# Kernel tuning notes

Measured on AMD Instinct MI355X. Metric: run time of the kernel, lower is better.

Reference implementation:

```python
import jax, jax.numpy as jnp
import numpy as np

B, L, D, H = 8, 512, 512, 8  # d_keys = d_values = d_model = D (default path)


def setup_inputs() -> dict:
    key = jax.random.key(0)
    ks = jax.random.split(key, 9)
    w = 0.02
    return {
        "queries": jax.random.normal(ks[0], (B, L, D), dtype=jnp.float32),
        "keys": jax.random.normal(ks[1], (B, L, D), dtype=jnp.float32),
        "values": jax.random.normal(ks[2], (B, L, D), dtype=jnp.float32),
        "Wq": jax.random.normal(ks[3], (D, D * H), dtype=jnp.float32) * w,
        "bq": jnp.zeros((D * H,), dtype=jnp.float32),
        "Wk": jax.random.normal(ks[4], (D, D * H), dtype=jnp.float32) * w,
        "bk": jnp.zeros((D * H,), dtype=jnp.float32),
        "Wv": jax.random.normal(ks[5], (D, D * H), dtype=jnp.float32) * w,
        "bv": jnp.zeros((D * H,), dtype=jnp.float32),
        "attn_mask": 0,  # must be falsy; original code would crash on a real tensor mask
    }


def reference(queries, keys, values, Wq, bq, Wk, bk, Wv, bv, attn_mask):
    b, l, d = queries.shape
    h = Wq.shape[1] // d
    # projections -> (B, L, H, E) with E = d_model
    q = (queries @ Wq + bq).reshape(b, l, h, d)
    k = (keys @ Wk + bk).reshape(b, l, h, d)
    v = (values @ Wv + bv).reshape(b, l, h, d)
    scale = 1.0 / np.sqrt(d).astype(np.float32)
    # per-position head-vs-head scores (B, L, H, H); equivalent to the i-loop
    s = jnp.einsum('blhe,blge->blhg', q, k) * scale
    p = jax.nn.softmax(s, axis=-1)
    # diagonal (l == i) contribution, summed over positions -> (B, H, E)
    attn_part = jnp.einsum('blhg,blge->bhe', p, v)
    # off-diagonal (l != i): uniform 1/H softmax of zero scores, (L-1) copies
    uniform_part = (jnp.float32(l - 1) / h) * v.sum(axis=(1, 2))  # (B, E)
    out = attn_part + uniform_part[:, None, :]  # (B, H, E)
    # final view(B, L, -1): requires L | H*E
    return out.reshape(b, l, -1)
```

## Files before the change

### kernel.cpp

```cpp
#include <hip/hip_runtime.h>


using bf16x8 = __attribute__((ext_vector_type(8))) short;
using f32x4  = __attribute__((ext_vector_type(4))) float;

__device__ __forceinline__ unsigned short f2bf(float f) {
    union { float f; unsigned int u; } c; c.f = f;
    unsigned int u = c.u;
    u += 0x7FFFu + ((u >> 16) & 1u);
    return (unsigned short)(u >> 16);
}
__device__ __forceinline__ float bflo(unsigned int u) {
    union { unsigned int u; float f; } c; c.u = u << 16; return c.f;
}
__device__ __forceinline__ float bfhi(unsigned int u) {
    union { unsigned int u; float f; } c; c.u = u & 0xFFFF0000u; return c.f;
}

#define GLOAD16(gp, lp) __builtin_amdgcn_global_load_lds( \
    (const __attribute__((address_space(1))) unsigned int*)(gp), \
    (__attribute__((address_space(3))) unsigned int*)(lp), 16, 0, 0)

__global__ __launch_bounds__(256) void prep(
    const float* __restrict__ x0, const float* __restrict__ x1,
    unsigned short* __restrict__ o0, unsigned short* __restrict__ o1,
    const float* __restrict__ w0, const float* __restrict__ w1,
    unsigned short* __restrict__ t0, unsigned short* __restrict__ t1)
{
    const int z = blockIdx.z;
    if (z < 2) {
        const float* src = (z == 0) ? x0 : x1;
        unsigned short* dst = (z == 0) ? o0 : o1;
        int i = (blockIdx.x * 256 + threadIdx.x) * 4;
        float4 v = *(const float4*)(src + i);
        ushort4 o;
        o.x = f2bf(v.x); o.y = f2bf(v.y); o.z = f2bf(v.z); o.w = f2bf(v.w);
        *(ushort4*)(dst + i) = o;
    } else {
        const float* W = (z == 2) ? w0 : w1;
        unsigned short* T = (z == 2) ? t0 : t1;
        __shared__ float tile[32][33];
        const int n0 = (blockIdx.x & 127) * 32, k0 = (blockIdx.x >> 7) * 32;
        const int tx = threadIdx.x & 31, ty = threadIdx.x >> 5;
        #pragma unroll
        for (int j = 0; j < 32; j += 8)
            tile[ty + j][tx] = W[(size_t)(k0 + ty + j) * 4096 + n0 + tx];
        __syncthreads();
        #pragma unroll
        for (int j = 0; j < 32; j += 8)
            T[(size_t)(n0 + ty + j) * 512 + k0 + tx] = f2bf(tile[tx][ty + j]);
    }
}

__global__ __launch_bounds__(512) void gemm_bt256(
    const unsigned short* __restrict__ a0, const unsigned short* __restrict__ a1,
    const unsigned short* __restrict__ w0, const unsigned short* __restrict__ w1,
    const float* __restrict__ b0, const float* __restrict__ b1,
    unsigned char* __restrict__ c0, unsigned char* __restrict__ c1)
{
    const unsigned short* A;  const unsigned short* Bt; const float* bias; unsigned char* C;
    if (blockIdx.z == 0) { A = a0; Bt = w0; bias = b0; C = c0; }
    else                 { A = a1; Bt = w1; bias = b1; C = c1; }

    __shared__ __align__(16) unsigned short SH[65536];

    const int tid  = threadIdx.x;
    const int lane = tid & 63;
    const int wid  = tid >> 6;
    const int wr   = wid >> 2;
    const int wn   = wid & 3;
    const int linb = blockIdx.y * 16 + blockIdx.x;
    const int swz  = (linb & 7) * 32 + (linb >> 3);
    const int bx   = (swz >> 6) * 4 + (swz & 3);
    const int by   = (swz >> 2) & 15;
    const int row0 = by * 256;
    const int n0   = bx * 256;
    const int sgran = (lane & 7) ^ (lane >> 3);

    const int swb0 = (((lane >> 4)    ) ^ (lane & 7)) << 4;
    const int swb1 = (((lane >> 4) | 4) ^ (lane & 7)) << 4;
    const char* bA0 = (const char*)SH + (wr * 128 + (lane & 15)) * 128 + swb0;
    const char* bA1 = (const char*)SH + (wr * 128 + (lane & 15)) * 128 + swb1;
    const char* bB0 = (const char*)SH + 65536 + (wn * 64 + (lane & 15)) * 128 + swb0;
    const char* bB1 = (const char*)SH + 65536 + (wn * 64 + (lane & 15)) * 128 + swb1;

#define LD_A(c, m, s) (*(const bf16x8*)(((s) ? bA1 : bA0) + (c) * 32768 + (m) * 2048))
#define LD_B(c, n, s) (*(const bf16x8*)(((s) ? bB1 : bB0) + (c) * 32768 + (n) * 2048))

    const unsigned short* gA = A  + (size_t)(row0 + wid * 8 + (lane >> 3)) * 512 + sgran * 8;
    const unsigned short* gB = Bt + (size_t)(n0   + wid * 8 + (lane >> 3)) * 512 + sgran * 8;

#define STAGE_A(gp, buf, half, trel)                                              \
    {                                                                             \
        GLOAD16((gp) + ((half) * 128      ) * 512 + (trel) * 64,                  \
                SH + (buf) * 16384 + ((half) * 128      + wid * 8) * 64);         \
        GLOAD16((gp) + ((half) * 128 + 64 ) * 512 + (trel) * 64,                  \
                SH + (buf) * 16384 + ((half) * 128 + 64 + wid * 8) * 64);         \
    }
#define STAGE_B(gp, buf, half, trel)                                              \
    {                                                                             \
        GLOAD16((gp) + ((half) * 128      ) * 512 + (trel) * 64,                  \
                SH + 32768 + (buf) * 16384 + ((half) * 128      + wid * 8) * 64); \
        GLOAD16((gp) + ((half) * 128 + 64 ) * 512 + (trel) * 64,                  \
                SH + 32768 + (buf) * 16384 + ((half) * 128 + 64 + wid * 8) * 64); \
    }

#define BAR() __builtin_amdgcn_s_barrier()
#define VMC4() asm volatile("s_waitcnt vmcnt(4)" ::: "memory")
#define VMC0() asm volatile("s_waitcnt vmcnt(0)" ::: "memory")

    f32x4 acc[8][4];
    #pragma unroll
    for (int m = 0; m < 8; ++m)
        #pragma unroll
        for (int n = 0; n < 4; ++n)
            acc[m][n] = (f32x4){0.f, 0.f, 0.f, 0.f};

    bf16x8 bfr[4][2];
    bf16x8 fa0, fa1, fa2, fa3;

#define LDA_Q(c, q) { fa0 = LD_A(c, 2*(q), 0); fa1 = LD_A(c, 2*(q), 1);           \
                      fa2 = LD_A(c, 2*(q)+1, 0); fa3 = LD_A(c, 2*(q)+1, 1); }
#define LDB_ALL(c) { _Pragma("unroll") for (int n = 0; n < 4; ++n) {              \
                       bfr[n][0] = LD_B(c, n, 0); bfr[n][1] = LD_B(c, n, 1); } }
#define MFMA_Q(q) { __builtin_amdgcn_s_setprio(1);                                \
    _Pragma("unroll") for (int n = 0; n < 4; ++n) {                               \
      acc[2*(q)][n]   = __builtin_amdgcn_mfma_f32_16x16x32_bf16(bfr[n][0], fa0, acc[2*(q)][n],   0,0,0); \
      acc[2*(q)][n]   = __builtin_amdgcn_mfma_f32_16x16x32_bf16(bfr[n][1], fa1, acc[2*(q)][n],   0,0,0); \
      acc[2*(q)+1][n] = __builtin_amdgcn_mfma_f32_16x16x32_bf16(bfr[n][0], fa2, acc[2*(q)+1][n], 0,0,0); \
      acc[2*(q)+1][n] = __builtin_amdgcn_mfma_f32_16x16x32_bf16(bfr[n][1], fa3, acc[2*(q)+1][n], 0,0,0); } \
    __builtin_amdgcn_s_setprio(0); }

    STAGE_B(gB, 0, 0, 0); STAGE_B(gB, 0, 1, 0);
    STAGE_A(gA, 0, 0, 0); STAGE_A(gA, 0, 1, 0);
    STAGE_B(gB, 1, 0, 1); STAGE_B(gB, 1, 1, 1);
    VMC4();
    BAR();

    const unsigned short* gAt = gA;
    const unsigned short* gBt = gB;
    for (int i = 0; i < 4; ++i) {
        const bool s23 = (i < 3);

        LDA_Q(0, 0); LDB_ALL(0);
        STAGE_A(gAt, 1, 0, 1);
        BAR(); MFMA_Q(0); BAR();

        LDA_Q(0, 1);
        STAGE_A(gAt, 1, 1, 1);
        BAR(); MFMA_Q(1); BAR();

        LDA_Q(0, 2);
        if (s23) STAGE_B(gBt, 0, 0, 2);
        BAR(); MFMA_Q(2); BAR();

        LDA_Q(0, 3);
        if (s23) STAGE_B(gBt, 0, 1, 2);
        BAR(); MFMA_Q(3);
        if (s23) { VMC4(); } else { VMC0(); }
        BAR();

        LDA_Q(1, 0); LDB_ALL(1);
        if (s23) STAGE_A(gAt, 0, 0, 2);
        BAR(); MFMA_Q(0); BAR();

        LDA_Q(1, 1);
        if (s23) STAGE_A(gAt, 0, 1, 2);
        BAR(); MFMA_Q(1); BAR();

        LDA_Q(1, 2);
        if (s23) STAGE_B(gBt, 1, 0, 3);
        BAR(); MFMA_Q(2); BAR();

        LDA_Q(1, 3);
        if (s23) STAGE_B(gBt, 1, 1, 3);
        BAR(); MFMA_Q(3);
        if (s23) { VMC4(); }
        BAR();

        gAt += 128; gBt += 128;
    }

    {
        const int q  = lane >> 4;
        const int tr = wr * 128 + (lane & 15);
        unsigned char* SB = (unsigned char*)SH;
        #pragma unroll
        for (int n = 0; n < 4; ++n) {
            float4 bb = *(const float4*)(bias + n0 + wn * 64 + n * 16 + q * 4);
            const int g16 = wn * 4 + n;
            #pragma unroll
            for (int m = 0; m < 8; ++m) {
                const int trm = tr + m * 16;
                unsigned int pk = __builtin_amdgcn_cvt_pk_fp8_f32(
                    acc[m][n][0] + bb.x, acc[m][n][1] + bb.y, 0u, false);
                pk = __builtin_amdgcn_cvt_pk_fp8_f32(
                    acc[m][n][2] + bb.z, acc[m][n][3] + bb.w, pk, true);
                *(unsigned int*)(SB + trm * 256 + ((g16 ^ (trm & 15)) << 4) + q * 4) = pk;
            }
        }
        BAR();
        #pragma unroll
        for (int it = 0; it < 8; ++it) {
            const int f = it * 512 + tid;
            const int rr = f >> 4, gg = f & 15;
            uint4 v = *(const uint4*)(SB + rr * 256 + ((gg ^ (rr & 15)) << 4));
            *(uint4*)(C + (size_t)(row0 + rr) * 4096 + gg * 16 + n0) = v;
        }
    }
#undef STAGE_A
#undef STAGE_B
#undef LD_A
#undef LD_B
}

__global__ __launch_bounds__(256) void mfscores(const unsigned char* __restrict__ Q,
                                                const unsigned char* __restrict__ K,
                                                float* __restrict__ P,
                                                float* __restrict__ pbpart)
{
    __shared__ float Pl[8 * 64];
    const int b = blockIdx.x, lc = blockIdx.y;
    const int tid = threadIdx.x, lane = tid & 63, w = tid >> 6;
    const int l0 = lc * 8;

    const int colr = lane & 15;
    const int ko   = lane >> 4;
    const int la   = l0 + w * 2 + (colr >> 3);
    const int hh   = colr & 7;
    const unsigned char* qrow = Q + (size_t)(b * 512 + la) * 4096 + hh * 512 + ko * 8;
    const unsigned char* krow = K + (size_t)(b * 512 + la) * 4096 + hh * 512 + ko * 8;

    f32x4 acc = (f32x4){0.f, 0.f, 0.f, 0.f};
    #pragma unroll
    for (int kt = 0; kt < 16; ++kt) {
        long long av = *(const long long*)(qrow + kt * 32);
        long long bv = *(const long long*)(krow + kt * 32);
        acc = __builtin_amdgcn_mfma_f32_16x16x32_fp8_fp8(av, bv, acc, 0, 0, 0);
    }

    const int lpr = ko >> 1;
    const int lpc = (lane >> 3) & 1;
    #pragma unroll
    for (int r = 0; r < 4; ++r) {
        float s = acc[r] * 0.04419417382415922f;
        float m = s;
        m = fmaxf(m, __shfl_xor(m, 1));
        m = fmaxf(m, __shfl_xor(m, 2));
        m = fmaxf(m, __shfl_xor(m, 4));
        float e = __expf(s - m);
        float ss = e;
        ss += __shfl_xor(ss, 1);
        ss += __shfl_xor(ss, 2);
        ss += __shfl_xor(ss, 4);
        float p = e / ss + 63.875f;
        if (lpr == lpc)
            Pl[(w * 2 + lpr) * 64 + ((ko & 1) * 4 + r) * 8 + (lane & 7)] = p;
    }
    __syncthreads();

    {
        const int l = tid >> 5, off = (tid & 31) * 2;
        float2 v = *(const float2*)&Pl[l * 64 + off];
        *(float2*)(P + (size_t)(b * 512 + l0 + l) * 64 + off) = v;
    }
    if (tid < 64) {
        float s = 0.f;
        #pragma unroll
        for (int l = 0; l < 8; ++l) s += Pl[l * 64 + tid];
        pbpart[((size_t)b * 64 + lc) * 64 + tid] = s;
    }
}

__global__ __launch_bounds__(256) void ykern(const float* __restrict__ P,
                                             const float* __restrict__ Xv,
                                             float* __restrict__ ypart)
{
    __shared__ float Pl[128 * 64];
    __shared__ float Xl[128 * 64];
    const int b = blockIdx.x, dt = blockIdx.y, lc = blockIdx.z;
    const int tid = threadIdx.x;
    const int tm = tid & 15, te = tid >> 4;

    const float* Pg = P + ((size_t)b * 512 + lc * 128) * 64;
    #pragma unroll
    for (int i = 0; i < 8; ++i)
        *(float4*)&Pl[(i * 256 + tid) * 4] = *(const float4*)(Pg + (size_t)(i * 256 + tid) * 4);
    const float* Xg = Xv + ((size_t)b * 512 + lc * 128) * 512 + dt * 64;
    #pragma unroll
    for (int i = 0; i < 8; ++i) {
        int flat = i * 256 + tid;
        int r = flat >> 4, q = flat & 15;
        *(float4*)&Xl[r * 64 + q * 4] = *(const float4*)(Xg + (size_t)r * 512 + q * 4);
    }
    __syncthreads();

    float4 acc[4];
    #pragma unroll
    for (int i = 0; i < 4; ++i) acc[i] = make_float4(0.f, 0.f, 0.f, 0.f);

    for (int l = 0; l < 128; ++l) {
        float4 pv = *(const float4*)&Pl[l * 64 + tm * 4];
        float4 xv = *(const float4*)&Xl[l * 64 + te * 4];
        acc[0].x += pv.x * xv.x; acc[0].y += pv.x * xv.y; acc[0].z += pv.x * xv.z; acc[0].w += pv.x * xv.w;
        acc[1].x += pv.y * xv.x; acc[1].y += pv.y * xv.y; acc[1].z += pv.y * xv.z; acc[1].w += pv.y * xv.w;
        acc[2].x += pv.z * xv.x; acc[2].y += pv.z * xv.y; acc[2].z += pv.z * xv.z; acc[2].w += pv.z * xv.w;
        acc[3].x += pv.w * xv.x; acc[3].y += pv.w * xv.y; acc[3].z += pv.w * xv.z; acc[3].w += pv.w * xv.w;
    }
    #pragma unroll
    for (int i = 0; i < 4; ++i)
        *(float4*)&ypart[(((size_t)lc * 8 + b) * 64 + tm * 4 + i) * 512 + dt * 64 + te * 4] = acc[i];
}

__global__ __launch_bounds__(256) void vgemm(const float* __restrict__ ypart,
                                             const float* __restrict__ Wv,
                                             float* __restrict__ partial)
{
    __shared__ float Al[64 * 64];
    __shared__ float Bl[64 * 64];
    const int et = blockIdx.x, kc = blockIdx.y;
    const int g = kc >> 3, d0 = (kc & 7) * 64, e0 = et * 64;
    const int tid = threadIdx.x;
    const int tm = tid & 15, te = tid >> 4;

    #pragma unroll
    for (int i = 0; i < 4; ++i) {
        int flat = i * 256 + tid;
        int bh = flat >> 4, dq = flat & 15;
        int yrow = (bh >> 3) * 64 + (bh & 7) * 8 + g;
        size_t base = ((size_t)(yrow >> 6) * 64 + (yrow & 63)) * 512 + d0 + dq * 4;
        float4 v = *(const float4*)(ypart + base);
        #pragma unroll
        for (int lc = 1; lc < 4; ++lc) {
            float4 t = *(const float4*)(ypart + (size_t)lc * 262144 + base);
            v.x += t.x; v.y += t.y; v.z += t.z; v.w += t.w;
        }
        *(float4*)&Al[bh * 64 + ((dq ^ (bh >> 2)) << 2)] = v;
    }
    #pragma unroll
    for (int i = 0; i < 4; ++i) {
        int flat = i * 256 + tid;
        int kk = flat >> 4, eq = flat & 15;
        *(float4*)&Bl[kk * 64 + eq * 4] =
            *(const float4*)(Wv + (size_t)(d0 + kk) * 4096 + g * 512 + e0 + eq * 4);
    }
    __syncthreads();

    float4 acc[4];
    #pragma unroll
    for (int j = 0; j < 4; ++j) acc[j] = make_float4(0.f, 0.f, 0.f, 0.f);

    for (int k = 0; k < 64; ++k) {
        float4 b4 = *(const float4*)&Bl[k * 64 + te * 4];
        const int gcol = (((k >> 2) ^ tm) << 2) + (k & 3);
        #pragma unroll
        for (int j = 0; j < 4; ++j) {
            float a = Al[(tm * 4 + j) * 64 + gcol];
            acc[j].x += a * b4.x; acc[j].y += a * b4.y;
            acc[j].z += a * b4.z; acc[j].w += a * b4.w;
        }
    }
    #pragma unroll
    for (int j = 0; j < 4; ++j)
        *(float4*)&partial[(size_t)kc * 32768 + (tm * 4 + j) * 512 + e0 + te * 4] = acc[j];
}

__global__ __launch_bounds__(256) void finalize(const float* __restrict__ partial,
                                                const float* __restrict__ pbpart,
                                                const float* __restrict__ bv,
                                                float* __restrict__ out)
{
    __shared__ float csh[8];
    const int blk = blockIdx.x;
    const int tid = threadIdx.x;
    const int b = blk >> 4, h = (blk >> 1) & 7;
    const int e = (blk & 1) * 256 + tid;

    if (tid < 8) {
        float s = 0.f;
        #pragma unroll 8
        for (int lcc = 0; lcc < 64; ++lcc)
            s += pbpart[((size_t)b * 64 + lcc) * 64 + h * 8 + tid];
        csh[tid] = s;
    }
    __syncthreads();

    const int i = ((b * 8 + h) << 9) + e;
    float s = 0.f;
    #pragma unroll
    for (int kc = 0; kc < 64; ++kc) s += partial[(size_t)kc * 32768 + i];
    float bt = 0.f;
    #pragma unroll
    for (int g = 0; g < 8; ++g) bt += csh[g] * bv[g * 512 + e];
    out[i] = s + bt;
}

extern "C" void kernel_launch(void* const* d_in, const int* in_sizes, int n_in,
                              void* d_out, int out_size, void* d_ws, size_t ws_size,
                              hipStream_t stream)
{
    const float* queries = (const float*)d_in[0];
    const float* keys    = (const float*)d_in[1];
    const float* values  = (const float*)d_in[2];
    const float* Wq      = (const float*)d_in[3];
    const float* bq      = (const float*)d_in[4];
    const float* Wk      = (const float*)d_in[5];
    const float* bk      = (const float*)d_in[6];
    const float* Wv      = (const float*)d_in[7];
    const float* bv      = (const float*)d_in[8];

    unsigned short* xq  = (unsigned short*)d_ws;
    unsigned short* xk  = xq  + (1u << 21);
    unsigned short* wtq = xk  + (1u << 21);
    unsigned short* wtk = wtq + (1u << 21);
    unsigned char*  Q   = (unsigned char*)(wtk + (1u << 21));
    unsigned char*  Kb  = Q + (1u << 24);
    float* P      = (float*)(Kb + (1u << 24));
    float* pbpart = P + 262144;
    float* ypart  = pbpart + 32768;
    float* part   = ypart + 4 * 262144;

    prep<<<dim3(2048, 1, 4), 256, 0, stream>>>(queries, keys, xq, xk, Wq, Wk, wtq, wtk);
    gemm_bt256<<<dim3(16, 16, 2), 512, 0, stream>>>(xq, xk, wtq, wtk, bq, bk, Q, Kb);
    mfscores<<<dim3(8, 64), 256, 0, stream>>>(Q, Kb, P, pbpart);
    ykern<<<dim3(8, 8, 4), 256, 0, stream>>>(P, values, ypart);
    vgemm<<<dim3(8, 64), 256, 0, stream>>>(ypart, Wv, part);
    finalize<<<dim3(128), 256, 0, stream>>>(part, pbpart, bv, (float*)d_out);
}
```

Baseline: 84.74 us.

## Switch Q/K projection GEMM inputs from bf16 to scaled fp8

Converts the query/key activations and transposed weights to fp8 instead of bf16, with the weights prescaled by 16. The projection GEMM now uses fp8 MFMA, half-size LDS tiles, fewer staged loads and a new swizzle, and its launch bounds add an occupancy hint. Bias and the score scale are adjusted to cancel the 16x factor. This halves GEMM input bandwidth and raises MFMA throughput, at the cost of more quantization error in the Q and K projections.

```diff
diff --git a/kernel.cpp b/kernel.cpp
--- a/kernel.cpp
+++ b/kernel.cpp
@@ -1,20 +1,10 @@
 #include <hip/hip_runtime.h>
 
 
-using bf16x8 = __attribute__((ext_vector_type(8))) short;
-using f32x4  = __attribute__((ext_vector_type(4))) float;
-
-__device__ __forceinline__ unsigned short f2bf(float f) {
-    union { float f; unsigned int u; } c; c.f = f;
-    unsigned int u = c.u;
-    u += 0x7FFFu + ((u >> 16) & 1u);
-    return (unsigned short)(u >> 16);
-}
+using f32x4 = __attribute__((ext_vector_type(4))) float;
+
 __device__ __forceinline__ float bflo(unsigned int u) {
     union { unsigned int u; float f; } c; c.u = u << 16; return c.f;
-}
-__device__ __forceinline__ float bfhi(unsigned int u) {
-    union { unsigned int u; float f; } c; c.u = u & 0xFFFF0000u; return c.f;
 }
 
 #define GLOAD16(gp, lp) __builtin_amdgcn_global_load_lds( \
@@ -23,22 +13,28 @@
 
 __global__ __launch_bounds__(256) void prep(
     const float* __restrict__ x0, const float* __restrict__ x1,
-    unsigned short* __restrict__ o0, unsigned short* __restrict__ o1,
+    unsigned char* __restrict__ o0, unsigned char* __restrict__ o1,
     const float* __restrict__ w0, const float* __restrict__ w1,
-    unsigned short* __restrict__ t0, unsigned short* __restrict__ t1)
+    unsigned char* __restrict__ t0, unsigned char* __restrict__ t1)
 {
     const int z = blockIdx.z;
     if (z < 2) {
         const float* src = (z == 0) ? x0 : x1;
-        unsigned short* dst = (z == 0) ? o0 : o1;
-        int i = (blockIdx.x * 256 + threadIdx.x) * 4;
-        float4 v = *(const float4*)(src + i);
-        ushort4 o;
-        o.x = f2bf(v.x); o.y = f2bf(v.y); o.z = f2bf(v.z); o.w = f2bf(v.w);
-        *(ushort4*)(dst + i) = o;
+        unsigned char* dst = (z == 0) ? o0 : o1;
+        int i = (blockIdx.x * 256 + threadIdx.x) * 8;
+        if (i < 2097152) {
+            float4 a = *(const float4*)(src + i);
+            float4 b = *(const float4*)(src + i + 4);
+            uint2 u;
+            u.x = __builtin_amdgcn_cvt_pk_fp8_f32(a.x, a.y, 0u, false);
+            u.x = __builtin_amdgcn_cvt_pk_fp8_f32(a.z, a.w, u.x, true);
+            u.y = __builtin_amdgcn_cvt_pk_fp8_f32(b.x, b.y, 0u, false);
+            u.y = __builtin_amdgcn_cvt_pk_fp8_f32(b.z, b.w, u.y, true);
+            *(uint2*)(dst + i) = u;
+        }
     } else {
         const float* W = (z == 2) ? w0 : w1;
-        unsigned short* T = (z == 2) ? t0 : t1;
+        unsigned char* T = (z == 2) ? t0 : t1;
         __shared__ float tile[32][33];
         const int n0 = (blockIdx.x & 127) * 32, k0 = (blockIdx.x >> 7) * 32;
         const int tx = threadIdx.x & 31, ty = threadIdx.x >> 5;
@@ -46,23 +42,26 @@
         for (int j = 0; j < 32; j += 8)
             tile[ty + j][tx] = W[(size_t)(k0 + ty + j) * 4096 + n0 + tx];
         __syncthreads();
-        #pragma unroll
-        for (int j = 0; j < 32; j += 8)
-            T[(size_t)(n0 + ty + j) * 512 + k0 + tx] = f2bf(tile[tx][ty + j]);
-    }
-}
-
-__global__ __launch_bounds__(512) void gemm_bt256(
-    const unsigned short* __restrict__ a0, const unsigned short* __restrict__ a1,
-    const unsigned short* __restrict__ w0, const unsigned short* __restrict__ w1,
+        const int n = ty * 4 + (tx >> 3), kq = tx & 7;
+        unsigned int pk = __builtin_amdgcn_cvt_pk_fp8_f32(
+            16.f * tile[kq * 4 + 0][n], 16.f * tile[kq * 4 + 1][n], 0u, false);
+        pk = __builtin_amdgcn_cvt_pk_fp8_f32(
+            16.f * tile[kq * 4 + 2][n], 16.f * tile[kq * 4 + 3][n], pk, true);
+        *(unsigned int*)(T + (size_t)(n0 + n) * 512 + k0 + kq * 4) = pk;
+    }
+}
+
+__global__ __launch_bounds__(512, 4) void gemm_bt256(
+    const unsigned char* __restrict__ a0, const unsigned char* __restrict__ a1,
+    const unsigned char* __restrict__ w0, const unsigned char* __restrict__ w1,
     const float* __restrict__ b0, const float* __restrict__ b1,
     unsigned char* __restrict__ c0, unsigned char* __restrict__ c1)
 {
-    const unsigned short* A;  const unsigned short* Bt; const float* bias; unsigned char* C;
+    const unsigned char* A;  const unsigned char* Bt; const float* bias; unsigned char* C;
     if (blockIdx.z == 0) { A = a0; Bt = w0; bias = b0; C = c0; }
     else                 { A = a1; Bt = w1; bias = b1; C = c1; }
 
-    __shared__ __align__(16) unsigned short SH[65536];
+    __shared__ __align__(16) unsigned char SH[65536];
 
     const int tid  = threadIdx.x;
     const int lane = tid & 63;
@@ -75,38 +74,30 @@
     const int by   = (swz >> 2) & 15;
     const int row0 = by * 256;
     const int n0   = bx * 256;
-    const int sgran = (lane & 7) ^ (lane >> 3);
-
-    const int swb0 = (((lane >> 4)    ) ^ (lane & 7)) << 4;
-    const int swb1 = (((lane >> 4) | 4) ^ (lane & 7)) << 4;
-    const char* bA0 = (const char*)SH + (wr * 128 + (lane & 15)) * 128 + swb0;
-    const char* bA1 = (const char*)SH + (wr * 128 + (lane & 15)) * 128 + swb1;
-    const char* bB0 = (const char*)SH + 65536 + (wn * 64 + (lane & 15)) * 128 + swb0;
-    const char* bB1 = (const char*)SH + 65536 + (wn * 64 + (lane & 15)) * 128 + swb1;
-
-#define LD_A(c, m, s) (*(const bf16x8*)(((s) ? bA1 : bA0) + (c) * 32768 + (m) * 2048))
-#define LD_B(c, n, s) (*(const bf16x8*)(((s) ? bB1 : bB0) + (c) * 32768 + (n) * 2048))
-
-    const unsigned short* gA = A  + (size_t)(row0 + wid * 8 + (lane >> 3)) * 512 + sgran * 8;
-    const unsigned short* gB = Bt + (size_t)(n0   + wid * 8 + (lane >> 3)) * 512 + sgran * 8;
+
+    const int sg4 = (lane & 3) ^ ((lane >> 2) & 3);
+    const unsigned char* gA = A  + (size_t)(row0 + wid * 16 + (lane >> 2)) * 512 + sg4 * 16;
+    const unsigned char* gB = Bt + (size_t)(n0   + wid * 16 + (lane >> 2)) * 512 + sg4 * 16;
 
 #define STAGE_A(gp, buf, half, trel)                                              \
-    {                                                                             \
-        GLOAD16((gp) + ((half) * 128      ) * 512 + (trel) * 64,                  \
-                SH + (buf) * 16384 + ((half) * 128      + wid * 8) * 64);         \
-        GLOAD16((gp) + ((half) * 128 + 64 ) * 512 + (trel) * 64,                  \
-                SH + (buf) * 16384 + ((half) * 128 + 64 + wid * 8) * 64);         \
-    }
+    GLOAD16((gp) + (half) * 128 * 512 + (trel) * 64,                              \
+            SH + (buf) * 16384 + ((half) * 128 + wid * 16) * 64)
 #define STAGE_B(gp, buf, half, trel)                                              \
-    {                                                                             \
-        GLOAD16((gp) + ((half) * 128      ) * 512 + (trel) * 64,                  \
-                SH + 32768 + (buf) * 16384 + ((half) * 128      + wid * 8) * 64); \
-        GLOAD16((gp) + ((half) * 128 + 64 ) * 512 + (trel) * 64,                  \
-                SH + 32768 + (buf) * 16384 + ((half) * 128 + 64 + wid * 8) * 64); \
-    }
+    GLOAD16((gp) + (half) * 128 * 512 + (trel) * 64,                              \
+            SH + 32768 + (buf) * 16384 + ((half) * 128 + wid * 16) * 64)
+
+    const int swo0 = ((((lane >> 5)    ) ^ (lane & 3)) << 4) + ((lane >> 4) & 1) * 8;
+    const int swo1 = (((2 + (lane >> 5)) ^ (lane & 3)) << 4) + ((lane >> 4) & 1) * 8;
+    const char* bA0 = (const char*)SH + (wr * 128 + (lane & 15)) * 64 + swo0;
+    const char* bA1 = (const char*)SH + (wr * 128 + (lane & 15)) * 64 + swo1;
+    const char* bB0 = (const char*)SH + 32768 + (wn * 64 + (lane & 15)) * 64 + swo0;
+    const char* bB1 = (const char*)SH + 32768 + (wn * 64 + (lane & 15)) * 64 + swo1;
+
+#define LD_A(c, m, s) (*(const long long*)(((s) ? bA1 : bA0) + (c) * 16384 + (m) * 1024))
+#define LD_B(c, n, s) (*(const long long*)(((s) ? bB1 : bB0) + (c) * 16384 + (n) * 1024))
 
 #define BAR() __builtin_amdgcn_s_barrier()
-#define VMC4() asm volatile("s_waitcnt vmcnt(4)" ::: "memory")
+#define VMC2() asm volatile("s_waitcnt vmcnt(2)" ::: "memory")
 #define VMC0() asm volatile("s_waitcnt vmcnt(0)" ::: "memory")
 
     f32x4 acc[8][4];
@@ -116,8 +107,8 @@
         for (int n = 0; n < 4; ++n)
             acc[m][n] = (f32x4){0.f, 0.f, 0.f, 0.f};
 
-    bf16x8 bfr[4][2];
-    bf16x8 fa0, fa1, fa2, fa3;
+    long long bfr[4][2];
+    long long fa0, fa1, fa2, fa3;
 
 #define LDA_Q(c, q) { fa0 = LD_A(c, 2*(q), 0); fa1 = LD_A(c, 2*(q), 1);           \
                       fa2 = LD_A(c, 2*(q)+1, 0); fa3 = LD_A(c, 2*(q)+1, 1); }
@@ -125,20 +116,20 @@
                        bfr[n][0] = LD_B(c, n, 0); bfr[n][1] = LD_B(c, n, 1); } }
 #define MFMA_Q(q) { __builtin_amdgcn_s_setprio(1);                                \
     _Pragma("unroll") for (int n = 0; n < 4; ++n) {                               \
-      acc[2*(q)][n]   = __builtin_amdgcn_mfma_f32_16x16x32_bf16(bfr[n][0], fa0, acc[2*(q)][n],   0,0,0); \
-      acc[2*(q)][n]   = __builtin_amdgcn_mfma_f32_16x16x32_bf16(bfr[n][1], fa1, acc[2*(q)][n],   0,0,0); \
-      acc[2*(q)+1][n] = __builtin_amdgcn_mfma_f32_16x16x32_bf16(bfr[n][0], fa2, acc[2*(q)+1][n], 0,0,0); \
-      acc[2*(q)+1][n] = __builtin_amdgcn_mfma_f32_16x16x32_bf16(bfr[n][1], fa3, acc[2*(q)+1][n], 0,0,0); } \
+      acc[2*(q)][n]   = __builtin_amdgcn_mfma_f32_16x16x32_fp8_fp8(bfr[n][0], fa0, acc[2*(q)][n],   0,0,0); \
+      acc[2*(q)][n]   = __builtin_amdgcn_mfma_f32_16x16x32_fp8_fp8(bfr[n][1], fa1, acc[2*(q)][n],   0,0,0); \
+      acc[2*(q)+1][n] = __builtin_amdgcn_mfma_f32_16x16x32_fp8_fp8(bfr[n][0], fa2, acc[2*(q)+1][n], 0,0,0); \
+      acc[2*(q)+1][n] = __builtin_amdgcn_mfma_f32_16x16x32_fp8_fp8(bfr[n][1], fa3, acc[2*(q)+1][n], 0,0,0); } \
     __builtin_amdgcn_s_setprio(0); }
 
     STAGE_B(gB, 0, 0, 0); STAGE_B(gB, 0, 1, 0);
     STAGE_A(gA, 0, 0, 0); STAGE_A(gA, 0, 1, 0);
     STAGE_B(gB, 1, 0, 1); STAGE_B(gB, 1, 1, 1);
-    VMC4();
+    VMC2();
     BAR();
 
-    const unsigned short* gAt = gA;
-    const unsigned short* gBt = gB;
+    const unsigned char* gAt = gA;
+    const unsigned char* gBt = gB;
     for (int i = 0; i < 4; ++i) {
         const bool s23 = (i < 3);
 
@@ -157,7 +148,7 @@
         LDA_Q(0, 3);
         if (s23) STAGE_B(gBt, 0, 1, 2);
         BAR(); MFMA_Q(3);
-        if (s23) { VMC4(); } else { VMC0(); }
+        if (s23) { VMC2(); } else { VMC0(); }
         BAR();
 
         LDA_Q(1, 0); LDB_ALL(1);
@@ -175,7 +166,7 @@
         LDA_Q(1, 3);
         if (s23) STAGE_B(gBt, 1, 1, 3);
         BAR(); MFMA_Q(3);
-        if (s23) { VMC4(); }
+        if (s23) { VMC2(); }
         BAR();
 
         gAt += 128; gBt += 128;
@@ -184,7 +175,6 @@
     {
         const int q  = lane >> 4;
         const int tr = wr * 128 + (lane & 15);
-        unsigned char* SB = (unsigned char*)SH;
         #pragma unroll
         for (int n = 0; n < 4; ++n) {
             float4 bb = *(const float4*)(bias + n0 + wn * 64 + n * 16 + q * 4);
@@ -193,10 +183,10 @@
             for (int m = 0; m < 8; ++m) {
                 const int trm = tr + m * 16;
                 unsigned int pk = __builtin_amdgcn_cvt_pk_fp8_f32(
-                    acc[m][n][0] + bb.x, acc[m][n][1] + bb.y, 0u, false);
+                    acc[m][n][0] + 16.f * bb.x, acc[m][n][1] + 16.f * bb.y, 0u, false);
                 pk = __builtin_amdgcn_cvt_pk_fp8_f32(
-                    acc[m][n][2] + bb.z, acc[m][n][3] + bb.w, pk, true);
-                *(unsigned int*)(SB + trm * 256 + ((g16 ^ (trm & 15)) << 4) + q * 4) = pk;
+                    acc[m][n][2] + 16.f * bb.z, acc[m][n][3] + 16.f * bb.w, pk, true);
+                *(unsigned int*)(SH + trm * 256 + ((g16 ^ (trm & 15)) << 4) + q * 4) = pk;
             }
         }
         BAR();
@@ -204,7 +194,7 @@
         for (int it = 0; it < 8; ++it) {
             const int f = it * 512 + tid;
             const int rr = f >> 4, gg = f & 15;
-            uint4 v = *(const uint4*)(SB + rr * 256 + ((gg ^ (rr & 15)) << 4));
+            uint4 v = *(const uint4*)(SH + rr * 256 + ((gg ^ (rr & 15)) << 4));
             *(uint4*)(C + (size_t)(row0 + rr) * 4096 + gg * 16 + n0) = v;
         }
     }
@@ -243,7 +233,7 @@
     const int lpc = (lane >> 3) & 1;
     #pragma unroll
     for (int r = 0; r < 4; ++r) {
-        float s = acc[r] * 0.04419417382415922f;
+        float s = acc[r] * 1.7263349150062e-4f;
         float m = s;
         m = fmaxf(m, __shfl_xor(m, 1));
         m = fmaxf(m, __shfl_xor(m, 2));
@@ -409,12 +399,12 @@
     const float* Wv      = (const float*)d_in[7];
     const float* bv      = (const float*)d_in[8];
 
-    unsigned short* xq  = (unsigned short*)d_ws;
-    unsigned short* xk  = xq  + (1u << 21);
-    unsigned short* wtq = xk  + (1u << 21);
-    unsigned short* wtk = wtq + (1u << 21);
-    unsigned char*  Q   = (unsigned char*)(wtk + (1u << 21));
-    unsigned char*  Kb  = Q + (1u << 24);
+    unsigned char* xq  = (unsigned char*)d_ws;
+    unsigned char* xk  = xq  + (1u << 21);
+    unsigned char* wtq = xk  + (1u << 21);
+    unsigned char* wtk = wtq + (1u << 21);
+    unsigned char* Q   = wtk + (1u << 21);
+    unsigned char* Kb  = Q   + (1u << 24);
     float* P      = (float*)(Kb + (1u << 24));
     float* pbpart = P + 262144;
     float* ypart  = pbpart + 32768;
```

After: 195.8 us. +131.1%, slower.
